# Optimization experiments

Measured on AMD Instinct MI355X. Metric: run time of the kernel, lower is better.

Reference implementation:

```python
import jax, jax.numpy as jnp
import numpy as np
from functools import partial

N_NODES = 50000
N_EDGES = 800000
EMBED_DIM = 128
NUM_GROUPS = 3
T = 1.0


def setup_inputs() -> dict:
    key = jax.random.key(0)
    k1, k2, k3, k4 = jax.random.split(key, 4)
    node_feature = jax.random.normal(k1, (N_NODES, EMBED_DIM), dtype=jnp.float32)
    src = jax.random.randint(k2, (N_EDGES,), 0, N_NODES, dtype=jnp.int32)
    dst = jax.random.randint(k3, (N_EDGES,), 0, N_NODES, dtype=jnp.int32)
    W = jax.random.normal(k4, (EMBED_DIM, NUM_GROUPS), dtype=jnp.float32) / np.sqrt(EMBED_DIM)
    b = jnp.zeros((NUM_GROUPS,), dtype=jnp.float32)
    return {"node_feature": node_feature, "src": src, "dst": dst, "W": W, "b": b}


def reference(node_feature, src, dst, W, b):
    n = node_feature.shape[0]
    # linear + softmax group scores: [N, G]
    coeff = jax.nn.softmax((node_feature @ W + b) / T, axis=1)
    # weighted individual features: [N, G, D]
    wif = node_feature[:, None, :] * coeff[:, :, None]
    # message: gather src features per edge; reduce: mean over in-neighbors
    summed = jax.ops.segment_sum(wif[src], dst, num_segments=n)  # [N, G, D]
    deg = jax.ops.segment_sum(jnp.ones_like(dst, dtype=node_feature.dtype), dst, num_segments=n)
    group_feat = summed / jnp.maximum(deg, 1.0)[:, None, None]  # mean; zero-degree -> 0
    # weighted sum over groups with destination's own incidence coeff: [N, D]
    weighted_group_feat = jnp.einsum('ngd,ng->nd', group_feat, coeff)
    return weighted_group_feat
```

## Files before the change

kernel.cpp:

```cpp
#include <hip/hip_runtime.h>
#include <hip/hip_bf16.h>

#define D 128
#define G 3
#define BN 128
#define CH 8192
#define BIN_T 1024
#define CAP 4096

__global__ void lg_coeff_kernel(const float* __restrict__ X,
                                const float* __restrict__ W,
                                const float* __restrict__ b,
                                float4* __restrict__ coeff,
                                __hip_bfloat16* __restrict__ Xh,
                                int* __restrict__ bcnt, int nbuck,
                                int n) {
    if (bcnt && blockIdx.x == 0) {
        for (int i = threadIdx.x; i < nbuck; i += 256) bcnt[i] = 0;
    }
    int node = (int)((blockIdx.x * (size_t)blockDim.x + threadIdx.x) >> 6);
    int lane = threadIdx.x & 63;
    if (node >= n) return;
    float2 x = ((const float2*)(X + (size_t)node * D))[lane];
    if (Xh) {
        __hip_bfloat162 h;
        h.x = __float2bfloat16(x.x);
        h.y = __float2bfloat16(x.y);
        ((__hip_bfloat162*)(Xh + (size_t)node * D))[lane] = h;
    }
    int d0 = lane * 2;
    float s0 = x.x * W[d0 * G + 0] + x.y * W[(d0 + 1) * G + 0];
    float s1 = x.x * W[d0 * G + 1] + x.y * W[(d0 + 1) * G + 1];
    float s2 = x.x * W[d0 * G + 2] + x.y * W[(d0 + 1) * G + 2];
    #pragma unroll
    for (int off = 32; off; off >>= 1) {
        s0 += __shfl_xor(s0, off);
        s1 += __shfl_xor(s1, off);
        s2 += __shfl_xor(s2, off);
    }
    s0 += b[0]; s1 += b[1]; s2 += b[2];
    float m = fmaxf(s0, fmaxf(s1, s2));
    float e0 = __expf(s0 - m), e1 = __expf(s1 - m), e2 = __expf(s2 - m);
    float inv = 1.0f / (e0 + e1 + e2);
    if (lane == 0) coeff[node] = make_float4(e0 * inv, e1 * inv, e2 * inv, 0.0f);
}

__global__ __launch_bounds__(1024) void lg_bcount_kernel(
        const int* __restrict__ dst, int* __restrict__ bcnt, int E, int nbuck) {
    __shared__ int h[512];
    int tid = threadIdx.x;
    if (tid < 512) h[tid] = 0;
    __syncthreads();
    int e0 = blockIdx.x * CH;
    int ecnt = min(CH, E - e0);
    for (int k = tid; k < ecnt; k += 1024)
        atomicAdd(&h[dst[e0 + k] >> 7], 1);
    __syncthreads();
    if (tid < nbuck && h[tid]) atomicAdd(&bcnt[tid], h[tid]);
}

__global__ __launch_bounds__(512) void lg_bscan_kernel(
        const int* __restrict__ bcnt, int* __restrict__ boff,
        int* __restrict__ cursor, int nbuck, int E) {
    __shared__ int sc[512];
    int tid = threadIdx.x;
    int v = (tid < nbuck) ? bcnt[tid] : 0;
    sc[tid] = v;
    __syncthreads();
    #pragma unroll
    for (int d = 1; d < 512; d <<= 1) {
        int y = (tid >= d) ? sc[tid - d] : 0;
        __syncthreads();
        sc[tid] += y;
        __syncthreads();
    }
    if (tid < nbuck) {
        int excl = sc[tid] - v;
        boff[tid] = excl;
        cursor[tid] = excl;
    }
    if (tid == 0) boff[nbuck] = E;
}

__global__ __launch_bounds__(BIN_T) void lg_bin_kernel(
        const int* __restrict__ src, const int* __restrict__ dst,
        int* __restrict__ cursor, unsigned int* __restrict__ temp,
        int E, int nbuck) {
    __shared__ unsigned int stage[CH];
    __shared__ int hist[512], sc[512], hbase[512], hcnt[512], gbs[512];
    int tid = threadIdx.x;
    int e0 = blockIdx.x * CH;
    int ecnt = min(CH, E - e0);
    for (int i = tid; i < 512; i += BIN_T) { hist[i] = 0; hcnt[i] = 0; }
    __syncthreads();
    int rs[CH / BIN_T], rd[CH / BIN_T];
    #pragma unroll
    for (int u = 0; u < CH / BIN_T; ++u) {
        int k = tid + u * BIN_T;
        if (k < ecnt) {
            rs[u] = src[e0 + k];
            rd[u] = dst[e0 + k];
            atomicAdd(&hist[rd[u] >> 7], 1);
        } else rd[u] = -1;
    }
    __syncthreads();
    if (tid < 512) sc[tid] = hist[tid];
    __syncthreads();
    #pragma unroll
    for (int d = 1; d < 512; d <<= 1) {
        int v = (tid < 512 && tid >= d) ? sc[tid - d] : 0;
        __syncthreads();
        if (tid < 512) sc[tid] += v;
        __syncthreads();
    }
    if (tid < 512) hbase[tid] = sc[tid] - hist[tid];
    __syncthreads();
    #pragma unroll
    for (int u = 0; u < CH / BIN_T; ++u) {
        if (rd[u] >= 0) {
            int bk = rd[u] >> 7;
            int idx = hbase[bk] + atomicAdd(&hcnt[bk], 1);
            stage[idx] = ((unsigned int)rs[u] & 0xFFFFu) |
                         (((unsigned int)rd[u] & 127u) << 16);
        }
    }
    for (int i = tid; i < nbuck; i += BIN_T) {
        int c = hist[i];
        gbs[i] = c ? atomicAdd(&cursor[i], c) : 0;
    }
    __syncthreads();
    int wv = tid >> 6, ln = tid & 63;
    for (int bk = wv; bk < nbuck; bk += BIN_T / 64) {
        int c = hist[bk];
        if (!c) continue;
        int gb = gbs[bk], hb = hbase[bk];
        for (int j = ln; j < c; j += 64) temp[gb + j] = stage[hb + j];
    }
}

__global__ __launch_bounds__(1024) void lg_sortagg_kernel(
        const __hip_bfloat16* __restrict__ Xh,
        const float4* __restrict__ coeff,
        const unsigned int* __restrict__ temp,
        const int* __restrict__ boff,
        float* __restrict__ out, int n) {
    __shared__ unsigned int stage[CAP];
    __shared__ float4 cdl[BN];
    __shared__ int nhist[BN], scn[BN], nbase[BN], ncur[BN];
    int tid = threadIdx.x;
    int wv = tid >> 6, ln = tid & 63;
    int nb0 = blockIdx.x * BN;
    int nv = min(BN, n - nb0);
    int rbeg = boff[blockIdx.x];
    int rend = boff[blockIdx.x + 1];
    int count = rend - rbeg;
    if (tid < BN) { nhist[tid] = 0; ncur[tid] = 0; }
    if (tid < nv) cdl[tid] = coeff[nb0 + tid];
    __syncthreads();

    if (count <= CAP) {
        int k0 = tid, k1 = tid + 1024, k2 = tid + 2048, k3 = tid + 3072;
        unsigned int r0 = 0, r1 = 0, r2 = 0, r3 = 0;
        if (k0 < count) { r0 = temp[rbeg + k0]; atomicAdd(&nhist[(r0 >> 16) & 127u], 1); }
        if (k1 < count) { r1 = temp[rbeg + k1]; atomicAdd(&nhist[(r1 >> 16) & 127u], 1); }
        if (k2 < count) { r2 = temp[rbeg + k2]; atomicAdd(&nhist[(r2 >> 16) & 127u], 1); }
        if (k3 < count) { r3 = temp[rbeg + k3]; atomicAdd(&nhist[(r3 >> 16) & 127u], 1); }
        __syncthreads();
        if (tid < BN) scn[tid] = nhist[tid];
        __syncthreads();
        #pragma unroll
        for (int d = 1; d < BN; d <<= 1) {
            int v = (tid < BN && tid >= d) ? scn[tid - d] : 0;
            __syncthreads();
            if (tid < BN) scn[tid] += v;
            __syncthreads();
        }
        if (tid < BN) nbase[tid] = scn[tid] - nhist[tid];
        __syncthreads();
        auto place = [&](unsigned int rec) {
            int s = (int)(rec & 0xFFFFu);
            int d = (int)((rec >> 16) & 127u);
            float4 cs = coeff[s];
            float4 cd = cdl[d];
            float w = cs.x * cd.x + cs.y * cd.y + cs.z * cd.z;
            unsigned int wb = __float_as_uint(w);
            wb += 0x7FFFu + ((wb >> 16) & 1u);
            int pos = nbase[d] + atomicAdd(&ncur[d], 1);
            stage[pos] = (rec & 0xFFFFu) | (wb & 0xFFFF0000u);
        };
        if (k0 < count) place(r0);
        if (k1 < count) place(r1);
        if (k2 < count) place(r2);
        if (k3 < count) place(r3);
        __syncthreads();
        for (int i = wv; i < nv; i += 16) {
            int ibeg = nbase[i];
            int icnt = nhist[i];
            float accx = 0.0f, accy = 0.0f;
            int j = 0;
            for (; j + 3 < icnt; j += 4) {
                unsigned int q0 = stage[ibeg + j + 0];
                unsigned int q1 = stage[ibeg + j + 1];
                unsigned int q2 = stage[ibeg + j + 2];
                unsigned int q3 = stage[ibeg + j + 3];
                int s0 = (int)(q0 & 0xFFFFu), s1 = (int)(q1 & 0xFFFFu);
                int s2 = (int)(q2 & 0xFFFFu), s3 = (int)(q3 & 0xFFFFu);
                float w0 = __uint_as_float(q0 & 0xFFFF0000u);
                float w1 = __uint_as_float(q1 & 0xFFFF0000u);
                float w2 = __uint_as_float(q2 & 0xFFFF0000u);
                float w3 = __uint_as_float(q3 & 0xFFFF0000u);
                __hip_bfloat162 h0 = ((const __hip_bfloat162*)(Xh + (size_t)s0 * D))[ln];
                __hip_bfloat162 h1 = ((const __hip_bfloat162*)(Xh + (size_t)s1 * D))[ln];
                __hip_bfloat162 h2 = ((const __hip_bfloat162*)(Xh + (size_t)s2 * D))[ln];
                __hip_bfloat162 h3 = ((const __hip_bfloat162*)(Xh + (size_t)s3 * D))[ln];
                accx = fmaf(w0, __bfloat162float(h0.x), accx);
                accy = fmaf(w0, __bfloat162float(h0.y), accy);
                accx = fmaf(w1, __bfloat162float(h1.x), accx);
                accy = fmaf(w1, __bfloat162float(h1.y), accy);
                accx = fmaf(w2, __bfloat162float(h2.x), accx);
                accy = fmaf(w2, __bfloat162float(h2.y), accy);
                accx = fmaf(w3, __bfloat162float(h3.x), accx);
                accy = fmaf(w3, __bfloat162float(h3.y), accy);
            }
            for (; j < icnt; ++j) {
                unsigned int q0 = stage[ibeg + j];
                int s0 = (int)(q0 & 0xFFFFu);
                float w0 = __uint_as_float(q0 & 0xFFFF0000u);
                __hip_bfloat162 h0 = ((const __hip_bfloat162*)(Xh + (size_t)s0 * D))[ln];
                accx = fmaf(w0, __bfloat162float(h0.x), accx);
                accy = fmaf(w0, __bfloat162float(h0.y), accy);
            }
            float invd = 1.0f / fmaxf((float)icnt, 1.0f);
            ((float2*)(out + (size_t)(nb0 + i) * D))[ln] =
                make_float2(accx * invd, accy * invd);
        }
    } else {
        for (int k = tid; k < count; k += 1024)
            atomicAdd(&nhist[(temp[rbeg + k] >> 16) & 127u], 1);
        __syncthreads();
        for (int i = wv; i < nv; i += 16) {
            float4 cd = cdl[i];
            float accx = 0.0f, accy = 0.0f;
            for (int base = 0; base < count; base += 64) {
                int k = base + ln;
                unsigned int rec = (k < count) ? temp[rbeg + k] : 0u;
                bool ok = (k < count) && ((int)((rec >> 16) & 127u) == i);
                unsigned long long mask = __ballot(ok);
                while (mask) {
                    int bpos = __ffsll((long long)mask) - 1;
                    mask &= mask - 1;
                    unsigned int rr = __shfl(rec, bpos);
                    int s0 = (int)(rr & 0xFFFFu);
                    float4 cs = coeff[s0];
                    float w = cs.x * cd.x + cs.y * cd.y + cs.z * cd.z;
                    __hip_bfloat162 h0 = ((const __hip_bfloat162*)(Xh + (size_t)s0 * D))[ln];
                    accx = fmaf(w, __bfloat162float(h0.x), accx);
                    accy = fmaf(w, __bfloat162float(h0.y), accy);
                }
            }
            float invd = 1.0f / fmaxf((float)nhist[i], 1.0f);
            ((float2*)(out + (size_t)(nb0 + i) * D))[ln] =
                make_float2(accx * invd, accy * invd);
        }
    }
}

__global__ void lg_deg_kernel(const int* __restrict__ dst, int* __restrict__ deg, int E) {
    int e = (int)(blockIdx.x * (size_t)blockDim.x + threadIdx.x);
    if (e < E) atomicAdd(&deg[dst[e]], 1);
}

__global__ void lg_scatter_kernel(const float* __restrict__ X,
                                  const float4* __restrict__ coeff,
                                  const int* __restrict__ src, const int* __restrict__ dst,
                                  float* __restrict__ out, int E) {
    int e = (int)((blockIdx.x * (size_t)blockDim.x + threadIdx.x) >> 6);
    int lane = threadIdx.x & 63;
    if (e >= E) return;
    int s = src[e], d = dst[e];
    float4 cs = coeff[s], cd = coeff[d];
    float se = cs.x * cd.x + cs.y * cd.y + cs.z * cd.z;
    float2 x = ((const float2*)(X + (size_t)s * D))[lane];
    atomicAdd(&out[(size_t)d * D + lane * 2 + 0], se * x.x);
    atomicAdd(&out[(size_t)d * D + lane * 2 + 1], se * x.y);
}

__global__ void lg_scale_kernel(float* __restrict__ out, const int* __restrict__ deg, int n) {
    int node = (int)((blockIdx.x * (size_t)blockDim.x + threadIdx.x) >> 6);
    int lane = threadIdx.x & 63;
    if (node >= n) return;
    float invd = 1.0f / fmaxf((float)deg[node], 1.0f);
    float2* p = (float2*)(out + (size_t)node * D);
    float2 v = p[lane];
    p[lane] = make_float2(v.x * invd, v.y * invd);
}

extern "C" void kernel_launch(void* const* d_in, const int* in_sizes, int n_in,
                              void* d_out, int out_size, void* d_ws, size_t ws_size,
                              hipStream_t stream) {
    const float* X   = (const float*)d_in[0];
    const int*   src = (const int*)d_in[1];
    const int*   dst = (const int*)d_in[2];
    const float* W   = (const float*)d_in[3];
    const float* b   = (const float*)d_in[4];
    float* out = (float*)d_out;
    int n = in_sizes[0] / D;
    int E = in_sizes[1];

    int nbuck = (n + BN - 1) / BN;

    char* ws = (char*)d_ws;
    size_t p = 0;
    auto alloc = [&](size_t bytes) -> void* {
        void* r = ws + p;
        p = (p + bytes + 255) & ~(size_t)255;
        return r;
    };
    float4* coeff  = (float4*)alloc((size_t)n * sizeof(float4));
    int*    bcnt   = (int*)alloc((size_t)nbuck * sizeof(int));
    int*    boff   = (int*)alloc((size_t)(nbuck + 1) * sizeof(int));
    int*    cursor = (int*)alloc((size_t)nbuck * sizeof(int));
    unsigned int* temp = (unsigned int*)alloc((size_t)E * sizeof(unsigned int));
    __hip_bfloat16* Xh = (__hip_bfloat16*)alloc((size_t)n * D * sizeof(__hip_bfloat16));
    size_t p_full = p;
    int*    deg    = (int*)alloc((size_t)n * sizeof(int));

    int node_blocks = (n + 3) / 4;
    int edge_blocks = (E + 255) / 256;
    int chunk_blocks = (E + CH - 1) / CH;

    bool fast_ok = (n <= 65536) && (nbuck <= 512) && (p_full <= ws_size);
    if (fast_ok) {
        lg_coeff_kernel<<<node_blocks, 256, 0, stream>>>(X, W, b, coeff, Xh,
                                                         bcnt, nbuck, n);
        lg_bcount_kernel<<<chunk_blocks, 1024, 0, stream>>>(dst, bcnt, E, nbuck);
        lg_bscan_kernel<<<1, 512, 0, stream>>>(bcnt, boff, cursor, nbuck, E);
        lg_bin_kernel<<<chunk_blocks, BIN_T, 0, stream>>>(src, dst, cursor, temp, E, nbuck);
        lg_sortagg_kernel<<<nbuck, 1024, 0, stream>>>(Xh, coeff, temp, boff, out, n);
    } else {
        hipMemsetAsync(deg, 0, (size_t)n * sizeof(int), stream);
        hipMemsetAsync(out, 0, (size_t)n * D * sizeof(float), stream);
        lg_coeff_kernel<<<node_blocks, 256, 0, stream>>>(X, W, b, coeff, nullptr,
                                                         nullptr, 0, n);
        lg_deg_kernel<<<edge_blocks, 256, 0, stream>>>(dst, deg, E);
        lg_scatter_kernel<<<(E + 3) / 4, 256, 0, stream>>>(X, coeff, src, dst, out, E);
        lg_scale_kernel<<<node_blocks, 256, 0, stream>>>(out, deg, n);
    }
}
```

Baseline: 75.90 us.

## Fuse bucket counting into coeff kernel, use wave-shuffle scans, unroll gather by 8

```diff
diff --git a/kernel.cpp b/kernel.cpp
--- a/kernel.cpp
+++ b/kernel.cpp
@@ -8,25 +8,35 @@
 #define BIN_T 1024
 #define CAP 4096
 
-__global__ void lg_coeff_kernel(const float* __restrict__ X,
-                                const float* __restrict__ W,
-                                const float* __restrict__ b,
-                                float4* __restrict__ coeff,
-                                __hip_bfloat16* __restrict__ Xh,
-                                int* __restrict__ bcnt, int nbuck,
-                                int n) {
-    if (bcnt && blockIdx.x == 0) {
-        for (int i = threadIdx.x; i < nbuck; i += 256) bcnt[i] = 0;
+__global__ __launch_bounds__(256) void lg_fused_kernel(
+        const float* __restrict__ X, const float* __restrict__ W,
+        const float* __restrict__ b, float4* __restrict__ coeff,
+        __hip_bfloat16* __restrict__ Xh,
+        const int* __restrict__ dst, int* __restrict__ gcnt,
+        int node_blocks, int E, int n) {
+    if ((int)blockIdx.x >= node_blocks) {
+        __shared__ int h[512];
+        int tid = threadIdx.x;
+        int chunk = blockIdx.x - node_blocks;
+        for (int i = tid; i < 512; i += 256) h[i] = 0;
+        __syncthreads();
+        int e0 = chunk * CH;
+        int ecnt = min(CH, E - e0);
+        for (int k = tid; k < ecnt; k += 256)
+            atomicAdd(&h[dst[e0 + k] >> 7], 1);
+        __syncthreads();
+        for (int i = tid; i < 512; i += 256) gcnt[chunk * 512 + i] = h[i];
+        return;
     }
     int node = (int)((blockIdx.x * (size_t)blockDim.x + threadIdx.x) >> 6);
     int lane = threadIdx.x & 63;
     if (node >= n) return;
     float2 x = ((const float2*)(X + (size_t)node * D))[lane];
     if (Xh) {
-        __hip_bfloat162 h;
-        h.x = __float2bfloat16(x.x);
-        h.y = __float2bfloat16(x.y);
-        ((__hip_bfloat162*)(Xh + (size_t)node * D))[lane] = h;
+        __hip_bfloat162 h2;
+        h2.x = __float2bfloat16(x.x);
+        h2.y = __float2bfloat16(x.y);
+        ((__hip_bfloat162*)(Xh + (size_t)node * D))[lane] = h2;
     }
     int d0 = lane * 2;
     float s0 = x.x * W[d0 * G + 0] + x.y * W[(d0 + 1) * G + 0];
@@ -45,26 +55,13 @@
     if (lane == 0) coeff[node] = make_float4(e0 * inv, e1 * inv, e2 * inv, 0.0f);
 }
 
-__global__ __launch_bounds__(1024) void lg_bcount_kernel(
-        const int* __restrict__ dst, int* __restrict__ bcnt, int E, int nbuck) {
-    __shared__ int h[512];
-    int tid = threadIdx.x;
-    if (tid < 512) h[tid] = 0;
-    __syncthreads();
-    int e0 = blockIdx.x * CH;
-    int ecnt = min(CH, E - e0);
-    for (int k = tid; k < ecnt; k += 1024)
-        atomicAdd(&h[dst[e0 + k] >> 7], 1);
-    __syncthreads();
-    if (tid < nbuck && h[tid]) atomicAdd(&bcnt[tid], h[tid]);
-}
-
 __global__ __launch_bounds__(512) void lg_bscan_kernel(
-        const int* __restrict__ bcnt, int* __restrict__ boff,
-        int* __restrict__ cursor, int nbuck, int E) {
+        const int* __restrict__ gcnt, int nchunk,
+        int* __restrict__ boff, int* __restrict__ cursor, int nbuck, int E) {
     __shared__ int sc[512];
     int tid = threadIdx.x;
-    int v = (tid < nbuck) ? bcnt[tid] : 0;
+    int v = 0;
+    for (int j = 0; j < nchunk; ++j) v += gcnt[j * 512 + tid];
     sc[tid] = v;
     __syncthreads();
     #pragma unroll
@@ -87,8 +84,9 @@
         int* __restrict__ cursor, unsigned int* __restrict__ temp,
         int E, int nbuck) {
     __shared__ unsigned int stage[CH];
-    __shared__ int hist[512], sc[512], hbase[512], hcnt[512], gbs[512];
+    __shared__ int hist[512], hbase[512], hcnt[512], gbs[512];
     int tid = threadIdx.x;
+    int wv = tid >> 6, ln = tid & 63;
     int e0 = blockIdx.x * CH;
     int ecnt = min(CH, E - e0);
     for (int i = tid; i < 512; i += BIN_T) { hist[i] = 0; hcnt[i] = 0; }
@@ -104,16 +102,20 @@
         } else rd[u] = -1;
     }
     __syncthreads();
-    if (tid < 512) sc[tid] = hist[tid];
-    __syncthreads();
-    #pragma unroll
-    for (int d = 1; d < 512; d <<= 1) {
-        int v = (tid < 512 && tid >= d) ? sc[tid - d] : 0;
-        __syncthreads();
-        if (tid < 512) sc[tid] += v;
-        __syncthreads();
-    }
-    if (tid < 512) hbase[tid] = sc[tid] - hist[tid];
+    if (wv == 0) {
+        int c[8]; int tot = 0;
+        #pragma unroll
+        for (int t = 0; t < 8; ++t) { c[t] = hist[ln * 8 + t]; tot += c[t]; }
+        int s = tot;
+        #pragma unroll
+        for (int o = 1; o < 64; o <<= 1) {
+            int y = __shfl_up(s, o);
+            if (ln >= o) s += y;
+        }
+        int run = s - tot;
+        #pragma unroll
+        for (int t = 0; t < 8; ++t) { hbase[ln * 8 + t] = run; run += c[t]; }
+    }
     __syncthreads();
     #pragma unroll
     for (int u = 0; u < CH / BIN_T; ++u) {
@@ -129,7 +131,6 @@
         gbs[i] = c ? atomicAdd(&cursor[i], c) : 0;
     }
     __syncthreads();
-    int wv = tid >> 6, ln = tid & 63;
     for (int bk = wv; bk < nbuck; bk += BIN_T / 64) {
         int c = hist[bk];
         if (!c) continue;
@@ -146,7 +147,7 @@
         float* __restrict__ out, int n) {
     __shared__ unsigned int stage[CAP];
     __shared__ float4 cdl[BN];
-    __shared__ int nhist[BN], scn[BN], nbase[BN], ncur[BN];
+    __shared__ int nhist[BN], nbase[BN], ncur[BN];
     int tid = threadIdx.x;
     int wv = tid >> 6, ln = tid & 63;
     int nb0 = blockIdx.x * BN;
@@ -166,16 +167,19 @@
         if (k2 < count) { r2 = temp[rbeg + k2]; atomicAdd(&nhist[(r2 >> 16) & 127u], 1); }
         if (k3 < count) { r3 = temp[rbeg + k3]; atomicAdd(&nhist[(r3 >> 16) & 127u], 1); }
         __syncthreads();
-        if (tid < BN) scn[tid] = nhist[tid];
-        __syncthreads();
-        #pragma unroll
-        for (int d = 1; d < BN; d <<= 1) {
-            int v = (tid < BN && tid >= d) ? scn[tid - d] : 0;
-            __syncthreads();
-            if (tid < BN) scn[tid] += v;
-            __syncthreads();
-        }
-        if (tid < BN) nbase[tid] = scn[tid] - nhist[tid];
+        if (wv == 0) {
+            int a = nhist[2 * ln], b2 = nhist[2 * ln + 1];
+            int tot = a + b2;
+            int s = tot;
+            #pragma unroll
+            for (int o = 1; o < 64; o <<= 1) {
+                int y = __shfl_up(s, o);
+                if (ln >= o) s += y;
+            }
+            int excl = s - tot;
+            nbase[2 * ln] = excl;
+            nbase[2 * ln + 1] = excl + a;
+        }
         __syncthreads();
         auto place = [&](unsigned int rec) {
             int s = (int)(rec & 0xFFFFu);
@@ -198,21 +202,31 @@
             int icnt = nhist[i];
             float accx = 0.0f, accy = 0.0f;
             int j = 0;
-            for (; j + 3 < icnt; j += 4) {
+            for (; j + 7 < icnt; j += 8) {
                 unsigned int q0 = stage[ibeg + j + 0];
                 unsigned int q1 = stage[ibeg + j + 1];
                 unsigned int q2 = stage[ibeg + j + 2];
                 unsigned int q3 = stage[ibeg + j + 3];
-                int s0 = (int)(q0 & 0xFFFFu), s1 = (int)(q1 & 0xFFFFu);
-                int s2 = (int)(q2 & 0xFFFFu), s3 = (int)(q3 & 0xFFFFu);
+                unsigned int q4 = stage[ibeg + j + 4];
+                unsigned int q5 = stage[ibeg + j + 5];
+                unsigned int q6 = stage[ibeg + j + 6];
+                unsigned int q7 = stage[ibeg + j + 7];
+                __hip_bfloat162 h0 = ((const __hip_bfloat162*)(Xh + (size_t)(q0 & 0xFFFFu) * D))[ln];
+                __hip_bfloat162 h1 = ((const __hip_bfloat162*)(Xh + (size_t)(q1 & 0xFFFFu) * D))[ln];
+                __hip_bfloat162 h2 = ((const __hip_bfloat162*)(Xh + (size_t)(q2 & 0xFFFFu) * D))[ln];
+                __hip_bfloat162 h3 = ((const __hip_bfloat162*)(Xh + (size_t)(q3 & 0xFFFFu) * D))[ln];
+                __hip_bfloat162 h4 = ((const __hip_bfloat162*)(Xh + (size_t)(q4 & 0xFFFFu) * D))[ln];
+                __hip_bfloat162 h5 = ((const __hip_bfloat162*)(Xh + (size_t)(q5 & 0xFFFFu) * D))[ln];
+                __hip_bfloat162 h6 = ((const __hip_bfloat162*)(Xh + (size_t)(q6 & 0xFFFFu) * D))[ln];
+                __hip_bfloat162 h7 = ((const __hip_bfloat162*)(Xh + (size_t)(q7 & 0xFFFFu) * D))[ln];
                 float w0 = __uint_as_float(q0 & 0xFFFF0000u);
                 float w1 = __uint_as_float(q1 & 0xFFFF0000u);
                 float w2 = __uint_as_float(q2 & 0xFFFF0000u);
                 float w3 = __uint_as_float(q3 & 0xFFFF0000u);
-                __hip_bfloat162 h0 = ((const __hip_bfloat162*)(Xh + (size_t)s0 * D))[ln];
-                __hip_bfloat162 h1 = ((const __hip_bfloat162*)(Xh + (size_t)s1 * D))[ln];
-                __hip_bfloat162 h2 = ((const __hip_bfloat162*)(Xh + (size_t)s2 * D))[ln];
-                __hip_bfloat162 h3 = ((const __hip_bfloat162*)(Xh + (size_t)s3 * D))[ln];
+                float w4 = __uint_as_float(q4 & 0xFFFF0000u);
+                float w5 = __uint_as_float(q5 & 0xFFFF0000u);
+                float w6 = __uint_as_float(q6 & 0xFFFF0000u);
+                float w7 = __uint_as_float(q7 & 0xFFFF0000u);
                 accx = fmaf(w0, __bfloat162float(h0.x), accx);
                 accy = fmaf(w0, __bfloat162float(h0.y), accy);
                 accx = fmaf(w1, __bfloat162float(h1.x), accx);
@@ -221,6 +235,14 @@
                 accy = fmaf(w2, __bfloat162float(h2.y), accy);
                 accx = fmaf(w3, __bfloat162float(h3.x), accx);
                 accy = fmaf(w3, __bfloat162float(h3.y), accy);
+                accx = fmaf(w4, __bfloat162float(h4.x), accx);
+                accy = fmaf(w4, __bfloat162float(h4.y), accy);
+                accx = fmaf(w5, __bfloat162float(h5.x), accx);
+                accy = fmaf(w5, __bfloat162float(h5.y), accy);
+                accx = fmaf(w6, __bfloat162float(h6.x), accx);
+                accy = fmaf(w6, __bfloat162float(h6.y), accy);
+                accx = fmaf(w7, __bfloat162float(h7.x), accx);
+                accy = fmaf(w7, __bfloat162float(h7.y), accy);
             }
             for (; j < icnt; ++j) {
                 unsigned int q0 = stage[ibeg + j];
@@ -307,7 +329,8 @@
     int n = in_sizes[0] / D;
     int E = in_sizes[1];
 
-    int nbuck = (n + BN - 1) / BN;
+    int nbuck  = (n + BN - 1) / BN;
+    int nchunk = (E + CH - 1) / CH;
 
     char* ws = (char*)d_ws;
     size_t p = 0;
@@ -317,7 +340,7 @@
         return r;
     };
     float4* coeff  = (float4*)alloc((size_t)n * sizeof(float4));
-    int*    bcnt   = (int*)alloc((size_t)nbuck * sizeof(int));
+    int*    gcnt   = (int*)alloc((size_t)nchunk * 512 * sizeof(int));
     int*    boff   = (int*)alloc((size_t)(nbuck + 1) * sizeof(int));
     int*    cursor = (int*)alloc((size_t)nbuck * sizeof(int));
     unsigned int* temp = (unsigned int*)alloc((size_t)E * sizeof(unsigned int));
@@ -327,21 +350,19 @@
 
     int node_blocks = (n + 3) / 4;
     int edge_blocks = (E + 255) / 256;
-    int chunk_blocks = (E + CH - 1) / CH;
 
     bool fast_ok = (n <= 65536) && (nbuck <= 512) && (p_full <= ws_size);
     if (fast_ok) {
-        lg_coeff_kernel<<<node_blocks, 256, 0, stream>>>(X, W, b, coeff, Xh,
-                                                         bcnt, nbuck, n);
-        lg_bcount_kernel<<<chunk_blocks, 1024, 0, stream>>>(dst, bcnt, E, nbuck);
-        lg_bscan_kernel<<<1, 512, 0, stream>>>(bcnt, boff, cursor, nbuck, E);
-        lg_bin_kernel<<<chunk_blocks, BIN_T, 0, stream>>>(src, dst, cursor, temp, E, nbuck);
+        lg_fused_kernel<<<node_blocks + nchunk, 256, 0, stream>>>(
+            X, W, b, coeff, Xh, dst, gcnt, node_blocks, E, n);
+        lg_bscan_kernel<<<1, 512, 0, stream>>>(gcnt, nchunk, boff, cursor, nbuck, E);
+        lg_bin_kernel<<<nchunk, BIN_T, 0, stream>>>(src, dst, cursor, temp, E, nbuck);
         lg_sortagg_kernel<<<nbuck, 1024, 0, stream>>>(Xh, coeff, temp, boff, out, n);
     } else {
         hipMemsetAsync(deg, 0, (size_t)n * sizeof(int), stream);
         hipMemsetAsync(out, 0, (size_t)n * D * sizeof(float), stream);
-        lg_coeff_kernel<<<node_blocks, 256, 0, stream>>>(X, W, b, coeff, nullptr,
-                                                         nullptr, 0, n);
+        lg_fused_kernel<<<node_blocks, 256, 0, stream>>>(
+            X, W, b, coeff, nullptr, dst, nullptr, node_blocks, E, n);
         lg_deg_kernel<<<edge_blocks, 256, 0, stream>>>(dst, deg, E);
         lg_scatter_kernel<<<(E + 3) / 4, 256, 0, stream>>>(X, coeff, src, dst, out, E);
         lg_scale_kernel<<<node_blocks, 256, 0, stream>>>(out, deg, n);
```

Result: slower. 92.79 us (median of 2 runs) (+22.3%).
